# Kernel optimization log

Hardware: AMD Instinct MI355X
Metric: run time of the kernel (lower is better)

The kernel has to match this reference:

```python
import jax, jax.numpy as jnp
from jax import lax
import numpy as np

B, DIM, HF, H, W, P = 4, 64, 128, 256, 256, 8  # patch_size = 8


def setup_inputs() -> dict:
    key = jax.random.key(0)
    k0, k1, k2, k3, k4 = jax.random.split(key, 5)
    C2 = 2 * HF
    x = jax.random.normal(k0, (B, DIM, H, W), dtype=jnp.float32)
    w_in = jax.random.normal(k1, (C2, DIM), dtype=jnp.float32) * 0.05      # 1x1 conv weight
    w_dw = jax.random.normal(k2, (C2, 1, 3, 3), dtype=jnp.float32) * 0.1   # depthwise 3x3
    fft_filt = 1.0 + 0.1 * jax.random.normal(k3, (C2, 1, 1, P, P // 2 + 1), dtype=jnp.float32)
    w_out = jax.random.normal(k4, (DIM, HF), dtype=jnp.float32) * 0.05     # 1x1 conv weight
    return {"x": x, "w_in": w_in, "w_dw": w_dw, "fft_filt": fft_filt, "w_out": w_out}


def reference(x, w_in, w_dw, fft_filt, w_out):
    # project_in: 1x1 conv (no bias)
    h = jnp.einsum('oc,bchw->bohw', w_in, x)
    b, c, hh, ww = h.shape
    # b c (h p1) (w p2) -> b c h w p1 p2
    hp = h.reshape(b, c, hh // P, P, ww // P, P).transpose(0, 1, 2, 4, 3, 5)
    # patchwise spectral gating
    f = jnp.fft.rfft2(hp.astype(jnp.float32)) * fft_filt
    hp = jnp.fft.irfft2(f, s=(P, P))
    # b c h w p1 p2 -> b c (h p1) (w p2)
    h = hp.transpose(0, 1, 2, 4, 3, 5).reshape(b, c, hh, ww)
    # depthwise 3x3 conv, SAME padding, groups = channels
    h = lax.conv_general_dilated(h, w_dw, (1, 1), 'SAME',
                                 feature_group_count=c,
                                 dimension_numbers=('NCHW', 'OIHW', 'NCHW'))
    x1, x2 = jnp.split(h, 2, axis=1)
    g = jax.nn.gelu(x1, approximate=False) * x2
    # project_out: 1x1 conv
    return jnp.einsum('oc,bchw->bohw', w_out, g)
```

## Files before the change

kernel.cpp:

```cpp
#include <hip/hip_runtime.h>
#include <hip/hip_bf16.h>

#define NB 4
#define DIMC 64
#define C2 256
#define HFC 128
#define HH 256
#define WW 256
#define HW (HH * WW)

typedef __attribute__((ext_vector_type(8))) short short8;
typedef __attribute__((ext_vector_type(4))) float f32x4;

__device__ __forceinline__ f32x4 mfma16(short8 a, short8 b, f32x4 c) {
  return __builtin_amdgcn_mfma_f32_16x16x32_bf16(a, b, c, 0, 0, 0);
}

__device__ __forceinline__ short f2bs(float f) {
  __hip_bfloat16 h = __float2bfloat16(f);
  union { __hip_bfloat16 h; short s; } u; u.h = h;
  return u.s;
}

__device__ __forceinline__ float bs2f(short s) {
  union { float f; unsigned u; } v;
  v.u = ((unsigned)(unsigned short)s) << 16;
  return v.f;
}

__device__ __forceinline__ float fast_gelu(float u) {
  float au = fabsf(u);
  float z = au * 0.70710678118654752f;
  float e = __expf(-z * z);
  float t = __builtin_amdgcn_rcpf(fmaf(0.3275911f, z, 1.0f));
  float p = fmaf(t, 1.061405429f, -1.453152027f);
  p = fmaf(t, p, 1.421413741f);
  p = fmaf(t, p, -0.284496736f);
  p = fmaf(t, p, 0.254829592f);
  p *= t;
  return fmaxf(u, 0.f) - 0.5f * au * p * e;
}

__global__ __launch_bounds__(64) void prep_kernel(
    const float* __restrict__ w_in, const float* __restrict__ fft,
    const float* __restrict__ w_out, __hip_bfloat16* __restrict__ A1,
    __hip_bfloat16* __restrict__ A2, __hip_bfloat16* __restrict__ Mf) {
  int blk = blockIdx.x;
  int l = threadIdx.x;
  int mm = l & 15, qj = l >> 4;
  if (blk < C2) {
    __shared__ float Feff[64];
    __shared__ float kc[64];
    __shared__ float ct[8];
    if (l < 8) {
      const float s = 0.70710678118654752f;
      const float v0[8] = {1.f, s, 0.f, -s, -1.f, -s, 0.f, s};
      ct[l] = v0[l];
    }
    int c = blk;
    const float* f = fft + c * 40;
    int u = l >> 3, v = l & 7;
    int um = (8 - u) & 7;
    float val;
    if (v <= 4) {
      val = f[u * 5 + v];
      if (v == 0 || v == 4) val = 0.5f * (val + f[um * 5 + v]);
    } else {
      val = f[um * 5 + (8 - v)];
    }
    Feff[l] = val;
    __syncthreads();
    int dy = l >> 3, dx = l & 7;
    float s = 0.f;
    for (int uu = 0; uu < 8; ++uu)
      for (int vv = 0; vv < 8; ++vv)
        s += Feff[uu * 8 + vv] * ct[(uu * dy + vv * dx) & 7];
    kc[l] = s * (1.f / 64.f);
    __syncthreads();
    for (int mb = 0; mb < 4; ++mb) {
      int p = mb * 16 + mm;
      int py = p >> 3, px = p & 7;
      for (int kb = 0; kb < 2; ++kb)
        for (int j = 0; j < 8; ++j) {
          int q = kb * 32 + qj * 8 + j;
          int qy = q >> 3, qx = q & 7;
          float kv = kc[((py - qy) & 7) * 8 + ((px - qx) & 7)];
          Mf[(size_t)c * 4096 + (size_t)((mb * 2 + kb) * 64 + l) * 8 + j] =
              __float2bfloat16(kv);
        }
    }
  } else if (blk == C2) {
    for (int mb = 0; mb < 16; ++mb)
      for (int kb = 0; kb < 2; ++kb)
        for (int j = 0; j < 8; ++j) {
          int m = mb * 16 + mm, k = kb * 32 + qj * 8 + j;
          A1[(size_t)((mb * 2 + kb) * 64 + l) * 8 + j] =
              __float2bfloat16(w_in[m * 64 + k]);
        }
  } else {
    for (int mb = 0; mb < 4; ++mb)
      for (int kb = 0; kb < 4; ++kb)
        for (int j = 0; j < 8; ++j) {
          int m = mb * 16 + mm, k = kb * 32 + qj * 8 + j;
          A2[(size_t)((mb * 4 + kb) * 64 + l) * 8 + j] =
              __float2bfloat16(w_out[m * 128 + k]);
        }
  }
}

__global__ __launch_bounds__(256) void gemm1_kernel(
    const float* __restrict__ x, const __hip_bfloat16* __restrict__ A1,
    __hip_bfloat16* __restrict__ h1) {
  __shared__ short Bt[8 * 64 * 8];
  int b = blockIdx.y;
  int n0 = blockIdx.x * 64;
  int t = threadIdx.x;
  int n = t & 63, dgrp = t >> 6;
  int nblk = n >> 4, nn = n & 15;
  const float* xb = x + (size_t)b * DIMC * HW + n0 + n;
#pragma unroll
  for (int s = 0; s < 2; ++s) {
    int jb = dgrp + s * 4;
    int kb = jb >> 2, quad = jb & 3;
    short8 pk;
#pragma unroll
    for (int j = 0; j < 8; ++j) pk[j] = f2bs(xb[(size_t)(jb * 8 + j) * HW]);
    *reinterpret_cast<short8*>(&Bt[((kb * 4 + nblk) * 64 + quad * 16 + nn) * 8]) = pk;
  }
  __syncthreads();
  int w = t >> 6, l = t & 63;
  const short8* A1v = reinterpret_cast<const short8*>(A1);
  short8 af[4][2];
#pragma unroll
  for (int mb = 0; mb < 4; ++mb)
#pragma unroll
    for (int kb = 0; kb < 2; ++kb)
      af[mb][kb] = A1v[((w * 4 + mb) * 2 + kb) * 64 + l];
  const short8* Bv = reinterpret_cast<const short8*>(Bt);
  f32x4 acc[4][4];
#pragma unroll
  for (int i = 0; i < 4; ++i)
#pragma unroll
    for (int j = 0; j < 4; ++j) acc[i][j] = (f32x4){0.f, 0.f, 0.f, 0.f};
#pragma unroll
  for (int nb = 0; nb < 4; ++nb) {
    short8 b0 = Bv[(0 * 4 + nb) * 64 + l];
    short8 b1 = Bv[(1 * 4 + nb) * 64 + l];
#pragma unroll
    for (int mb = 0; mb < 4; ++mb) {
      acc[mb][nb] = mfma16(af[mb][0], b0, acc[mb][nb]);
      acc[mb][nb] = mfma16(af[mb][1], b1, acc[mb][nb]);
    }
  }
  int quad = l >> 4, ln = l & 15;
#pragma unroll
  for (int mb = 0; mb < 4; ++mb)
#pragma unroll
    for (int nb = 0; nb < 4; ++nb)
#pragma unroll
      for (int r = 0; r < 4; ++r) {
        int m = w * 64 + mb * 16 + quad * 4 + r;
        int pix = n0 + nb * 16 + ln;
        h1[((size_t)b * C2 + m) * HW + pix] = __float2bfloat16(acc[mb][nb][r]);
      }
}

__global__ __launch_bounds__(256) void spectral_kernel(
    __hip_bfloat16* hb, const __hip_bfloat16* __restrict__ Mf) {
  int c = blockIdx.y;
  int t0 = blockIdx.x * 256;
  int tid = threadIdx.x;
  int w = tid >> 6, l = tid & 63;
  int quad = l >> 4, ln = l & 15;
  const short8* Mv = reinterpret_cast<const short8*>(Mf + (size_t)c * 4096);
  short8 af[4][2];
#pragma unroll
  for (int mb = 0; mb < 4; ++mb)
#pragma unroll
    for (int kb = 0; kb < 2; ++kb) af[mb][kb] = Mv[(mb * 2 + kb) * 64 + l];
  f32x4 acc[4][4];
#pragma unroll
  for (int i = 0; i < 4; ++i)
#pragma unroll
    for (int j = 0; j < 4; ++j) acc[i][j] = (f32x4){0.f, 0.f, 0.f, 0.f};
#pragma unroll
  for (int nb = 0; nb < 4; ++nb) {
    int tp = t0 + w * 64 + nb * 16 + ln;
    int bb = tp >> 10, Py = (tp >> 5) & 31, Px = tp & 31;
    const __hip_bfloat16* base =
        hb + (((size_t)bb * C2 + c) * HH + Py * 8) * WW + Px * 8;
    short8 bf0 = *reinterpret_cast<const short8*>(base + (size_t)quad * WW);
    short8 bf1 = *reinterpret_cast<const short8*>(base + (size_t)(4 + quad) * WW);
#pragma unroll
    for (int mb = 0; mb < 4; ++mb) {
      acc[mb][nb] = mfma16(af[mb][0], bf0, acc[mb][nb]);
      acc[mb][nb] = mfma16(af[mb][1], bf1, acc[mb][nb]);
    }
  }
  __syncthreads();
#pragma unroll
  for (int nb = 0; nb < 4; ++nb) {
    int tp = t0 + w * 64 + nb * 16 + ln;
    int bb = tp >> 10, Py = (tp >> 5) & 31, Px = tp & 31;
    __hip_bfloat16* ob = hb + (((size_t)bb * C2 + c) * HH + Py * 8) * WW + Px * 8;
#pragma unroll
    for (int mb = 0; mb < 4; ++mb)
#pragma unroll
      for (int r = 0; r < 4; ++r) {
        int p = mb * 16 + quad * 4 + r;
        ob[(p >> 3) * WW + (p & 7)] = __float2bfloat16(acc[mb][nb][r]);
      }
  }
}

__global__ __launch_bounds__(256) void dwgelu_kernel(
    const __hip_bfloat16* __restrict__ h2, const float* __restrict__ w_dw,
    __hip_bfloat16* __restrict__ gf) {
  __shared__ short ldsJ[8 * 1024];
  int jb = blockIdx.x;
  int y0 = blockIdx.y * 4;
  int b = blockIdx.z;
  int t = threadIdx.x;
  int j = t >> 5, xg = t & 31;
  int x0 = xg * 8;
  int c1 = jb * 8 + j, c2 = c1 + HFC;
  const __hip_bfloat16* hbase = h2 + (size_t)b * C2 * HW;

  float wd1[9], wd2[9];
#pragma unroll
  for (int k = 0; k < 9; ++k) {
    wd1[k] = w_dw[c1 * 9 + k];
    wd2[k] = w_dw[c2 * 9 + k];
  }

  float acc1[4][8], acc2[4][8];
#pragma unroll
  for (int r = 0; r < 4; ++r)
#pragma unroll
    for (int i = 0; i < 8; ++i) { acc1[r][i] = 0.f; acc2[r][i] = 0.f; }

#pragma unroll
  for (int ir = -1; ir <= 4; ++ir) {
    int yy = y0 + ir;
    bool valid = (yy >= 0) && (yy < HH);
    float f1[10], f2[10];
    if (valid) {
      const __hip_bfloat16* r1 = hbase + ((size_t)c1 * HH + yy) * WW;
      const __hip_bfloat16* r2 = hbase + ((size_t)c2 * HH + yy) * WW;
      short8 v1 = *reinterpret_cast<const short8*>(r1 + x0);
      short8 v2 = *reinterpret_cast<const short8*>(r2 + x0);
#pragma unroll
      for (int i = 0; i < 8; ++i) { f1[i + 1] = bs2f(v1[i]); f2[i + 1] = bs2f(v2[i]); }
      f1[0] = (x0 > 0) ? __bfloat162float(r1[x0 - 1]) : 0.f;
      f2[0] = (x0 > 0) ? __bfloat162float(r2[x0 - 1]) : 0.f;
      f1[9] = (x0 + 8 < WW) ? __bfloat162float(r1[x0 + 8]) : 0.f;
      f2[9] = (x0 + 8 < WW) ? __bfloat162float(r2[x0 + 8]) : 0.f;
    } else {
#pragma unroll
      for (int i = 0; i < 10; ++i) { f1[i] = 0.f; f2[i] = 0.f; }
    }
#pragma unroll
    for (int dy = -1; dy <= 1; ++dy) {
      int r = ir - dy;
      if (r < 0 || r >= 4) continue;
      int ky = dy + 1;
#pragma unroll
      for (int i = 0; i < 8; ++i) {
        acc1[r][i] += f1[i] * wd1[ky * 3] + f1[i + 1] * wd1[ky * 3 + 1] +
                      f1[i + 2] * wd1[ky * 3 + 2];
        acc2[r][i] += f2[i] * wd2[ky * 3] + f2[i + 1] * wd2[ky * 3 + 1] +
                      f2[i + 2] * wd2[ky * 3 + 2];
      }
    }
  }

#pragma unroll
  for (int r = 0; r < 4; ++r) {
    short8 pk;
#pragma unroll
    for (int i = 0; i < 8; ++i) {
      float g = fast_gelu(acc1[r][i]);
      pk[i] = f2bs(g * acc2[r][i]);
    }
    *reinterpret_cast<short8*>(&ldsJ[j * 1024 + r * 256 + x0]) = pk;
  }
  __syncthreads();

  int kb = jb >> 2, quad = jb & 3;
  short8* gfv = reinterpret_cast<short8*>(gf) + (size_t)b * 1048576;
#pragma unroll
  for (int k = 0; k < 4; ++k) {
    short8 v;
#pragma unroll
    for (int j2 = 0; j2 < 8; ++j2) v[j2] = ldsJ[j2 * 1024 + k * 256 + t];
    int pix = (y0 + k) * WW + t;
    gfv[((size_t)(pix >> 4) * 4 + kb) * 64 + quad * 16 + (pix & 15)] = v;
  }
}

__global__ __launch_bounds__(256) void gemm2_kernel(
    const __hip_bfloat16* __restrict__ gf, const __hip_bfloat16* __restrict__ A2,
    float* __restrict__ out) {
  int b = blockIdx.y;
  int pix0 = blockIdx.x * 256;
  int tid = threadIdx.x;
  int w = tid >> 6, l = tid & 63;
  int quad = l >> 4, ln = l & 15;
  const short8* A2v = reinterpret_cast<const short8*>(A2);
  short8 af[4][4];
#pragma unroll
  for (int mb = 0; mb < 4; ++mb)
#pragma unroll
    for (int kb = 0; kb < 4; ++kb) af[mb][kb] = A2v[(mb * 4 + kb) * 64 + l];
  const short8* gv = reinterpret_cast<const short8*>(gf) + (size_t)b * 1048576;
  f32x4 acc[4][4];
#pragma unroll
  for (int i = 0; i < 4; ++i)
#pragma unroll
    for (int j = 0; j < 4; ++j) acc[i][j] = (f32x4){0.f, 0.f, 0.f, 0.f};
#pragma unroll
  for (int nb = 0; nb < 4; ++nb) {
    size_t pixblk = (size_t)blockIdx.x * 16 + w * 4 + nb;
    short8 bf[4];
#pragma unroll
    for (int kb = 0; kb < 4; ++kb) bf[kb] = gv[(pixblk * 4 + kb) * 64 + l];
#pragma unroll
    for (int mb = 0; mb < 4; ++mb)
#pragma unroll
      for (int kb = 0; kb < 4; ++kb)
        acc[mb][nb] = mfma16(af[mb][kb], bf[kb], acc[mb][nb]);
  }
#pragma unroll
  for (int mb = 0; mb < 4; ++mb)
#pragma unroll
    for (int nb = 0; nb < 4; ++nb)
#pragma unroll
      for (int r = 0; r < 4; ++r) {
        int o = mb * 16 + quad * 4 + r;
        int pix = pix0 + w * 64 + nb * 16 + ln;
        out[((size_t)b * DIMC + o) * HW + pix] = acc[mb][nb][r];
      }
}

extern "C" void kernel_launch(void* const* d_in, const int* in_sizes, int n_in,
                              void* d_out, int out_size, void* d_ws,
                              size_t ws_size, hipStream_t stream) {
  const float* x = (const float*)d_in[0];
  const float* w_in = (const float*)d_in[1];
  const float* w_dw = (const float*)d_in[2];
  const float* fft = (const float*)d_in[3];
  const float* w_out = (const float*)d_in[4];
  float* out = (float*)d_out;
  char* ws = (char*)d_ws;
  __hip_bfloat16* A1 = (__hip_bfloat16*)(ws);
  __hip_bfloat16* A2 = (__hip_bfloat16*)(ws + 32768);
  __hip_bfloat16* Mf = (__hip_bfloat16*)(ws + 49152);
  __hip_bfloat16* gf = (__hip_bfloat16*)(ws + 2146304);
  __hip_bfloat16* h = (__hip_bfloat16*)(ws + 69255168);

  prep_kernel<<<258, 64, 0, stream>>>(w_in, fft, w_out, A1, A2, Mf);
  gemm1_kernel<<<dim3(1024, NB), 256, 0, stream>>>(x, A1, h);
  spectral_kernel<<<dim3(16, C2), 256, 0, stream>>>(h, Mf);
  dwgelu_kernel<<<dim3(16, 64, NB), 256, 0, stream>>>(h, w_dw, gf);
  gemm2_kernel<<<dim3(256, NB), 256, 0, stream>>>(gf, A2, out);
}
```

Measured before the change: 297.4 us.

## Fuse project-in GEMM with patchwise spectral matmul via LDS staging

Merges gemm1 and spectral kernels into one fs_kernel. Each block loads an 8-row by 64-pixel strip of x into LDS once, then loops over 16-channel groups: it computes the project-in output into a swizzled LDS tile and immediately applies the per-channel 64x64 spectral matrix before writing h. This removes one full write and read of the 256-channel bf16 intermediate in global memory. In exchange it uses 80KB of dynamic LDS, only 512 blocks, two barriers per channel group, and reloads the spectral matrices per block.

```diff
diff --git a/kernel.cpp b/kernel.cpp
--- a/kernel.cpp
+++ b/kernel.cpp
@@ -108,108 +108,106 @@
   }
 }
 
-__global__ __launch_bounds__(256) void gemm1_kernel(
+#define FS_LDS_BYTES 81920
+
+__device__ __forceinline__ int hs_idx(int cL, int row, int patch, int qx) {
+  int p2 = patch ^ ((cL >> 2) << 1) ^ row;
+  return 32768 + cL * 512 + row * 64 + p2 * 8 + qx;
+}
+
+__global__ __launch_bounds__(256, 2) void fs_kernel(
     const float* __restrict__ x, const __hip_bfloat16* __restrict__ A1,
-    __hip_bfloat16* __restrict__ h1) {
-  __shared__ short Bt[8 * 64 * 8];
-  int b = blockIdx.y;
-  int n0 = blockIdx.x * 64;
+    const __hip_bfloat16* __restrict__ Mf, __hip_bfloat16* __restrict__ h) {
+  extern __shared__ char smem[];
+  short* lds = reinterpret_cast<short*>(smem);
+  int pg = blockIdx.x, b = blockIdx.y;
+  int Py = pg >> 2, x0 = (pg & 3) * 64;
   int t = threadIdx.x;
-  int n = t & 63, dgrp = t >> 6;
-  int nblk = n >> 4, nn = n & 15;
-  const float* xb = x + (size_t)b * DIMC * HW + n0 + n;
-#pragma unroll
-  for (int s = 0; s < 2; ++s) {
-    int jb = dgrp + s * 4;
-    int kb = jb >> 2, quad = jb & 3;
-    short8 pk;
-#pragma unroll
-    for (int j = 0; j < 8; ++j) pk[j] = f2bs(xb[(size_t)(jb * 8 + j) * HW]);
-    *reinterpret_cast<short8*>(&Bt[((kb * 4 + nblk) * 64 + quad * 16 + nn) * 8]) = pk;
+  int w = t >> 6, l = t & 63;
+  int g = l >> 4;
+  int nn16 = l & 15;
+
+  {
+    int n = t & 63, dgrp = t >> 6;
+    int nblk = n >> 4, nn = n & 15;
+#pragma unroll
+    for (int py = 0; py < 8; ++py) {
+      const float* xb =
+          x + (size_t)b * DIMC * HW + (size_t)(Py * 8 + py) * WW + x0 + n;
+#pragma unroll
+      for (int s = 0; s < 2; ++s) {
+        int jb = dgrp + s * 4;
+        int kb = jb >> 2, quad = jb & 3;
+        short8 pk;
+#pragma unroll
+        for (int j = 0; j < 8; ++j) pk[j] = f2bs(xb[(size_t)(jb * 8 + j) * HW]);
+        *reinterpret_cast<short8*>(
+            &lds[(size_t)(py * 512 + (kb * 4 + nblk) * 64 + quad * 16 + nn) * 8]) = pk;
+      }
+    }
   }
   __syncthreads();
-  int w = t >> 6, l = t & 63;
+
   const short8* A1v = reinterpret_cast<const short8*>(A1);
-  short8 af[4][2];
-#pragma unroll
-  for (int mb = 0; mb < 4; ++mb)
-#pragma unroll
-    for (int kb = 0; kb < 2; ++kb)
-      af[mb][kb] = A1v[((w * 4 + mb) * 2 + kb) * 64 + l];
-  const short8* Bv = reinterpret_cast<const short8*>(Bt);
-  f32x4 acc[4][4];
-#pragma unroll
-  for (int i = 0; i < 4; ++i)
-#pragma unroll
-    for (int j = 0; j < 4; ++j) acc[i][j] = (f32x4){0.f, 0.f, 0.f, 0.f};
-#pragma unroll
-  for (int nb = 0; nb < 4; ++nb) {
-    short8 b0 = Bv[(0 * 4 + nb) * 64 + l];
-    short8 b1 = Bv[(1 * 4 + nb) * 64 + l];
-#pragma unroll
-    for (int mb = 0; mb < 4; ++mb) {
-      acc[mb][nb] = mfma16(af[mb][0], b0, acc[mb][nb]);
-      acc[mb][nb] = mfma16(af[mb][1], b1, acc[mb][nb]);
-    }
-  }
-  int quad = l >> 4, ln = l & 15;
-#pragma unroll
-  for (int mb = 0; mb < 4; ++mb)
-#pragma unroll
-    for (int nb = 0; nb < 4; ++nb)
-#pragma unroll
-      for (int r = 0; r < 4; ++r) {
-        int m = w * 64 + mb * 16 + quad * 4 + r;
-        int pix = n0 + nb * 16 + ln;
-        h1[((size_t)b * C2 + m) * HW + pix] = __float2bfloat16(acc[mb][nb][r]);
-      }
-}
-
-__global__ __launch_bounds__(256) void spectral_kernel(
-    __hip_bfloat16* hb, const __hip_bfloat16* __restrict__ Mf) {
-  int c = blockIdx.y;
-  int t0 = blockIdx.x * 256;
-  int tid = threadIdx.x;
-  int w = tid >> 6, l = tid & 63;
-  int quad = l >> 4, ln = l & 15;
-  const short8* Mv = reinterpret_cast<const short8*>(Mf + (size_t)c * 4096);
-  short8 af[4][2];
-#pragma unroll
-  for (int mb = 0; mb < 4; ++mb)
-#pragma unroll
-    for (int kb = 0; kb < 2; ++kb) af[mb][kb] = Mv[(mb * 2 + kb) * 64 + l];
-  f32x4 acc[4][4];
-#pragma unroll
-  for (int i = 0; i < 4; ++i)
-#pragma unroll
-    for (int j = 0; j < 4; ++j) acc[i][j] = (f32x4){0.f, 0.f, 0.f, 0.f};
-#pragma unroll
-  for (int nb = 0; nb < 4; ++nb) {
-    int tp = t0 + w * 64 + nb * 16 + ln;
-    int bb = tp >> 10, Py = (tp >> 5) & 31, Px = tp & 31;
-    const __hip_bfloat16* base =
-        hb + (((size_t)bb * C2 + c) * HH + Py * 8) * WW + Px * 8;
-    short8 bf0 = *reinterpret_cast<const short8*>(base + (size_t)quad * WW);
-    short8 bf1 = *reinterpret_cast<const short8*>(base + (size_t)(4 + quad) * WW);
-#pragma unroll
-    for (int mb = 0; mb < 4; ++mb) {
-      acc[mb][nb] = mfma16(af[mb][0], bf0, acc[mb][nb]);
-      acc[mb][nb] = mfma16(af[mb][1], bf1, acc[mb][nb]);
-    }
-  }
-  __syncthreads();
-#pragma unroll
-  for (int nb = 0; nb < 4; ++nb) {
-    int tp = t0 + w * 64 + nb * 16 + ln;
-    int bb = tp >> 10, Py = (tp >> 5) & 31, Px = tp & 31;
-    __hip_bfloat16* ob = hb + (((size_t)bb * C2 + c) * HH + Py * 8) * WW + Px * 8;
-#pragma unroll
-    for (int mb = 0; mb < 4; ++mb)
-#pragma unroll
-      for (int r = 0; r < 4; ++r) {
-        int p = mb * 16 + quad * 4 + r;
-        ob[(p >> 3) * WW + (p & 7)] = __float2bfloat16(acc[mb][nb][r]);
-      }
+  const short8* Mfv = reinterpret_cast<const short8*>(Mf);
+  const short8* xv = reinterpret_cast<const short8*>(lds);
+
+  for (int i = 0; i < 16; ++i) {
+    short8 af0 = A1v[(i * 2 + 0) * 64 + l];
+    short8 af1 = A1v[(i * 2 + 1) * 64 + l];
+#pragma unroll
+    for (int py2 = 0; py2 < 2; ++py2) {
+      int py = w * 2 + py2;
+#pragma unroll
+      for (int nb = 0; nb < 4; ++nb) {
+        short8 b0 = xv[py * 512 + (0 * 4 + nb) * 64 + l];
+        short8 b1 = xv[py * 512 + (1 * 4 + nb) * 64 + l];
+        f32x4 acc = (f32x4){0.f, 0.f, 0.f, 0.f};
+        acc = mfma16(af0, b0, acc);
+        acc = mfma16(af1, b1, acc);
+        int xc = nb * 16 + nn16;
+#pragma unroll
+        for (int r = 0; r < 4; ++r) {
+          int cL = g * 4 + r;
+          lds[hs_idx(cL, py, xc >> 3, xc & 7)] = f2bs(acc[r]);
+        }
+      }
+    }
+    __syncthreads();
+
+    int p8 = l & 7;
+#pragma unroll
+    for (int k = 0; k < 4; ++k) {
+      int cL = w * 4 + k;
+      int c = i * 16 + cL;
+      short8 mf[8];
+#pragma unroll
+      for (int mb = 0; mb < 4; ++mb)
+#pragma unroll
+        for (int kb = 0; kb < 2; ++kb)
+          mf[mb * 2 + kb] = Mfv[(size_t)c * 512 + (mb * 2 + kb) * 64 + l];
+      short8 bs0 = *reinterpret_cast<const short8*>(&lds[hs_idx(cL, g, p8, 0)]);
+      short8 bs1 = *reinterpret_cast<const short8*>(&lds[hs_idx(cL, 4 + g, p8, 0)]);
+      f32x4 accs[4];
+#pragma unroll
+      for (int mb = 0; mb < 4; ++mb) {
+        accs[mb] = (f32x4){0.f, 0.f, 0.f, 0.f};
+        accs[mb] = mfma16(mf[mb * 2 + 0], bs0, accs[mb]);
+        accs[mb] = mfma16(mf[mb * 2 + 1], bs1, accs[mb]);
+      }
+      if (nn16 < 8) {
+        __hip_bfloat16* ob = h + ((size_t)(b * C2 + c)) * HW +
+                             (size_t)(Py * 8) * WW + x0 + nn16 * 8;
+#pragma unroll
+        for (int mb = 0; mb < 4; ++mb)
+#pragma unroll
+          for (int r = 0; r < 4; ++r) {
+            int p = mb * 16 + g * 4 + r;
+            ob[(p >> 3) * WW + (p & 7)] = __float2bfloat16(accs[mb][r]);
+          }
+      }
+    }
+    __syncthreads();
   }
 }
 
@@ -279,8 +277,8 @@
     short8 pk;
 #pragma unroll
     for (int i = 0; i < 8; ++i) {
-      float g = fast_gelu(acc1[r][i]);
-      pk[i] = f2bs(g * acc2[r][i]);
+      float gg = fast_gelu(acc1[r][i]);
+      pk[i] = f2bs(gg * acc2[r][i]);
     }
     *reinterpret_cast<short8*>(&ldsJ[j * 1024 + r * 256 + x0]) = pk;
   }
@@ -358,9 +356,16 @@
   __hip_bfloat16* gf = (__hip_bfloat16*)(ws + 2146304);
   __hip_bfloat16* h = (__hip_bfloat16*)(ws + 69255168);
 
+  static bool fs_attr_set = false;
+  if (!fs_attr_set) {
+    (void)hipFuncSetAttribute((const void*)fs_kernel,
+                              hipFuncAttributeMaxDynamicSharedMemorySize,
+                              FS_LDS_BYTES);
+    fs_attr_set = true;
+  }
+
   prep_kernel<<<258, 64, 0, stream>>>(w_in, fft, w_out, A1, A2, Mf);
-  gemm1_kernel<<<dim3(1024, NB), 256, 0, stream>>>(x, A1, h);
-  spectral_kernel<<<dim3(16, C2), 256, 0, stream>>>(h, Mf);
+  fs_kernel<<<dim3(128, NB), 256, FS_LDS_BYTES, stream>>>(x, A1, Mf, h);
   dwgelu_kernel<<<dim3(16, 64, NB), 256, 0, stream>>>(h, w_dw, gf);
   gemm2_kernel<<<dim3(256, NB), 256, 0, stream>>>(gf, A2, out);
 }
```

Result: slower. 313.6 us (+5.5%).
